# Kernel tuning notes

Measured on AMD Instinct MI355X. Metric: run time of the kernel, lower is better.

## Reference

```python
import jax, jax.numpy as jnp
import numpy as np

DIM = 1024
GROUP = 16
N_LIN = 18   # 6 blocks * 3 quantized linears
N_LN = 5
RANK = 32
BATCH = 32768


def _dequant(q, s):
    # q: [DIM, DIM] int values in [0,16); s: [DIM*DIM/GROUP] per-group scales
    w = (q.reshape(-1, GROUP).astype(jnp.float32) - 8.0) * s[:, None]
    return w.reshape(DIM, DIM)


def _qlora_linear(x, q, s, b, la, lb):
    # x: [N, DIM]; la: [RANK, DIM]; lb: [DIM, RANK]
    w = _dequant(q, s)
    base = x @ w.T + b
    lora = (x @ la.T) @ lb.T
    return base + lora


def _layernorm(x, g, b):
    m = jnp.mean(x, axis=-1, keepdims=True)
    v = jnp.var(x, axis=-1, keepdims=True)
    return (x - m) / jnp.sqrt(v + 1e-5) * g + b


def setup_inputs() -> dict:
    key = jax.random.key(0)
    ks = jax.random.split(key, 8)
    x = jax.random.normal(ks[0], (BATCH, DIM), dtype=jnp.float32)
    wq = jax.random.randint(ks[1], (N_LIN, DIM, DIM), 0, 16, dtype=jnp.int32)
    scales = jax.random.uniform(ks[2], (N_LIN, DIM * DIM // GROUP), dtype=jnp.float32) * 0.02 + 1e-3
    bias = jax.random.normal(ks[3], (N_LIN, DIM), dtype=jnp.float32) * 0.02
    lora_a = jax.random.normal(ks[4], (N_LIN, RANK, DIM), dtype=jnp.float32) * 0.05
    lora_b = jax.random.normal(ks[5], (N_LIN, DIM, RANK), dtype=jnp.float32) * 0.05
    gamma = jnp.ones((N_LN, DIM), dtype=jnp.float32)
    beta = jnp.zeros((N_LN, DIM), dtype=jnp.float32)
    return {"x": x, "wq": wq, "scales": scales, "bias": bias,
            "lora_a": lora_a, "lora_b": lora_b, "gamma": gamma, "beta": beta}


def reference(x, wq, scales, bias, lora_a, lora_b, gamma, beta):
    h = x.astype(jnp.float32)
    li = 0
    for blk in range(6):
        r = h
        for j in range(3):
            h = _qlora_linear(h, wq[li], scales[li], bias[li], lora_a[li], lora_b[li])
            li += 1
            if j < 2:
                h = jax.nn.relu(h)
        h = h + r
        if blk < 5:
            h = _layernorm(h, gamma[blk], beta[blk])
    return h
```

## Files before the change

### kernel.cpp

```cpp
#include <hip/hip_runtime.h>

typedef unsigned int u32;
typedef unsigned short u16;
typedef _Float16 f16;
typedef f16 f16x8 __attribute__((ext_vector_type(8)));
typedef float f32x4 __attribute__((ext_vector_type(4)));
typedef u16 u16x8 __attribute__((ext_vector_type(8)));

#define DIM 1024
#define BATCH 32768
#define RANK 32
#define NLIN 18

__device__ __forceinline__ u16 f2h(float f) {
    f16 h = (f16)f;
    return *(u16*)&h;
}
__device__ __forceinline__ float h2f(u16 u) {
    f16 h;
    *(u16*)&h = u;
    return (float)h;
}

__device__ __forceinline__ void gload16(const u16* g, u16* l) {
    __builtin_amdgcn_global_load_lds((__attribute__((address_space(1))) const void*)g,
                                     (__attribute__((address_space(3))) void*)l,
                                     16, 0, 0);
}

#define BAR()        __builtin_amdgcn_s_barrier()
#define SB0()        __builtin_amdgcn_sched_barrier(0)
#define ASM_VM0()    asm volatile("s_waitcnt vmcnt(0)" ::: "memory")
#define ASM_VM4()    asm volatile("s_waitcnt vmcnt(4)" ::: "memory")
#define ASM_VM8()    asm volatile("s_waitcnt vmcnt(8)" ::: "memory")
#define ASM_LG0()    asm volatile("s_waitcnt lgkmcnt(0)" ::: "memory")

__global__ __launch_bounds__(256) void build_weff(
    const int* __restrict__ wq, const float* __restrict__ scales,
    const float* __restrict__ la, const float* __restrict__ lb,
    u16* __restrict__ weff)
{
    const int rb = blockIdx.x;
    const int li = blockIdx.y;
    const int tid = threadIdx.x;
    const int row0 = rb * 16;
    const int* wqL = wq + (size_t)li * DIM * DIM;
    const float* sL = scales + (size_t)li * (DIM * DIM / 16);
    const float* laL = la + (size_t)li * RANK * DIM;
    const float* lbL = lb + (size_t)li * DIM * RANK;
    u16* wout = weff + (size_t)li * DIM * DIM;

    for (int kc = 0; kc < 4; ++kc) {
        const int k = kc * 256 + tid;
        float lar[RANK];
        #pragma unroll
        for (int r = 0; r < RANK; ++r) lar[r] = laL[r * DIM + k];
        const int ks = k >> 4;
        #pragma unroll
        for (int og = 0; og < 16; og += 4) {
            const int m0 = row0 + og;
            float a0 = ((float)wqL[(m0 + 0) * DIM + k] - 8.0f) * sL[((m0 + 0) << 6) + ks];
            float a1 = ((float)wqL[(m0 + 1) * DIM + k] - 8.0f) * sL[((m0 + 1) << 6) + ks];
            float a2 = ((float)wqL[(m0 + 2) * DIM + k] - 8.0f) * sL[((m0 + 2) << 6) + ks];
            float a3 = ((float)wqL[(m0 + 3) * DIM + k] - 8.0f) * sL[((m0 + 3) << 6) + ks];
            #pragma unroll
            for (int r = 0; r < RANK; ++r) {
                const float lv = lar[r];
                a0 += lbL[(m0 + 0) * RANK + r] * lv;
                a1 += lbL[(m0 + 1) * RANK + r] * lv;
                a2 += lbL[(m0 + 2) * RANK + r] * lv;
                a3 += lbL[(m0 + 3) * RANK + r] * lv;
            }
            wout[(m0 + 0) * DIM + k] = f2h(a0);
            wout[(m0 + 1) * DIM + k] = f2h(a1);
            wout[(m0 + 2) * DIM + k] = f2h(a2);
            wout[(m0 + 3) * DIM + k] = f2h(a3);
        }
    }
}

__global__ __launch_bounds__(256) void xcast(const float* __restrict__ x, u16* __restrict__ o) {
    size_t i = ((size_t)blockIdx.x * 256 + threadIdx.x) * 8;
    float4 a = *(const float4*)(x + i);
    float4 b = *(const float4*)(x + i + 4);
    u16x8 v;
    v[0] = f2h(a.x); v[1] = f2h(a.y); v[2] = f2h(a.z); v[3] = f2h(a.w);
    v[4] = f2h(b.x); v[5] = f2h(b.y); v[6] = f2h(b.z); v[7] = f2h(b.w);
    *(u16x8*)(o + i) = v;
}

template<int EPI>
__global__ __launch_bounds__(512, 2) void gemm256(
    const u16* __restrict__ X, const u16* __restrict__ W,
    const float* __restrict__ bias, const u16* __restrict__ res,
    void* __restrict__ outp)
{
    __shared__ __align__(16) u16 As3[3 * 16384];
    __shared__ __align__(16) u16 Bs[2 * 16384];
    const int tid = threadIdx.x;
    const int bid = blockIdx.x;
    const int wg = (bid & 7) * 64 + (bid >> 3);
    const int bm = wg >> 2;
    const int bn = wg & 3;
    const int wid = tid >> 6;
    const int lane = tid & 63;
    const int wm = wid >> 2;
    const int wn = wid & 3;

    const int c1 = tid, c2 = tid + 512;
    const int r1 = c1 >> 3, r2 = c2 >> 3;
    const int l1 = ((c1 & 7) ^ (r1 & 7)) * 8;
    const int l2 = ((c2 & 7) ^ (r2 & 7)) * 8;
    const u16* gA0a = X + (size_t)(bm * 256 +       r1) * DIM + l1;
    const u16* gA0b = X + (size_t)(bm * 256 +       r2) * DIM + l2;
    const u16* gA1a = X + (size_t)(bm * 256 + 128 + r1) * DIM + l1;
    const u16* gA1b = X + (size_t)(bm * 256 + 128 + r2) * DIM + l2;
    const u16* gB0a = W + (size_t)(bn * 256 +       r1) * DIM + l1;
    const u16* gB0b = W + (size_t)(bn * 256 +       r2) * DIM + l2;
    const u16* gB1a = W + (size_t)(bn * 256 + 128 + r1) * DIM + l1;
    const u16* gB1b = W + (size_t)(bn * 256 + 128 + r2) * DIM + l2;
    const int d1 = c1 * 8, d2 = c2 * 8;

    const int kg = lane >> 4;
    const int sw = lane & 7;
    const int ch0 = ((0 * 4 + kg) ^ sw) * 8;
    const int ch1 = ((1 * 4 + kg) ^ sw) * 8;
    const int aoff = (wm * 128 + (lane & 15)) * 64;
    const int boff = (wn * 64 + (lane & 15)) * 64;

    f32x4 acc[8][4];
    #pragma unroll
    for (int i = 0; i < 8; ++i)
        #pragma unroll
        for (int j = 0; j < 4; ++j)
            acc[i][j] = (f32x4){0.f, 0.f, 0.f, 0.f};
    f16x8 af[4][2];
    f16x8 bf[4][2];

    gload16(gA0a, &As3[d1]);        gload16(gA0b, &As3[d2]);
    gload16(gA1a, &As3[8192 + d1]); gload16(gA1b, &As3[8192 + d2]);
    gload16(gB0a, &Bs[d1]);         gload16(gB0b, &Bs[d2]);
    gload16(gB1a, &Bs[8192 + d1]);  gload16(gB1b, &Bs[8192 + d2]);
    gload16(gA0a + 64, &As3[16384 + d1]);        gload16(gA0b + 64, &As3[16384 + d2]);
    gload16(gA1a + 64, &As3[16384 + 8192 + d1]); gload16(gA1b + 64, &As3[16384 + 8192 + d2]);
    gload16(gB0a + 64, &Bs[16384 + d1]);         gload16(gB0b + 64, &Bs[16384 + d2]);
    gload16(gB1a + 64, &Bs[16384 + 8192 + d1]);  gload16(gB1b + 64, &Bs[16384 + 8192 + d2]);

    #define RD_A(MH, BUF) { \
        _Pragma("unroll") \
        for (int fm = 0; fm < 4; ++fm) { \
            af[fm][0] = *(const f16x8*)&(BUF)[aoff + ((MH)*64 + fm*16)*64 + ch0]; \
            af[fm][1] = *(const f16x8*)&(BUF)[aoff + ((MH)*64 + fm*16)*64 + ch1]; \
        } }
    #define RD_B(BUF) { \
        _Pragma("unroll") \
        for (int fn = 0; fn < 4; ++fn) { \
            bf[fn][0] = *(const f16x8*)&(BUF)[boff + (fn*16)*64 + ch0]; \
            bf[fn][1] = *(const f16x8*)&(BUF)[boff + (fn*16)*64 + ch1]; \
        } }
    #define QUAD(MH, NH) { \
        __builtin_amdgcn_s_setprio(1); \
        _Pragma("unroll") \
        for (int ks = 0; ks < 2; ++ks) \
            _Pragma("unroll") \
            for (int fm = 0; fm < 4; ++fm) \
                _Pragma("unroll") \
                for (int fn = 0; fn < 2; ++fn) \
                    acc[(MH)*4+fm][(NH)*2+fn] = __builtin_amdgcn_mfma_f32_16x16x32_f16( \
                        af[fm][ks], bf[(NH)*2+fn][ks], acc[(MH)*4+fm][(NH)*2+fn], 0, 0, 0); \
        __builtin_amdgcn_s_setprio(0); }

    ASM_VM8();
    BAR();
    RD_A(0, (&As3[0]));
    RD_B((&Bs[0]));

    int aCur = 0, aNext = 16384, aWr = 32768;
    int bCur = 0, bNext = 16384;
    #pragma unroll 1
    for (int t = 0; t < 16; ++t) {
        const int ko2 = (t + 2) * 64;
        if (t <= 13) {
            gload16(gA0a + ko2, &As3[aWr + d1]);        gload16(gA0b + ko2, &As3[aWr + d2]);
            gload16(gA1a + ko2, &As3[aWr + 8192 + d1]); gload16(gA1b + ko2, &As3[aWr + 8192 + d2]);
        }
        ASM_LG0(); SB0();
        QUAD(0, 0); QUAD(0, 1);
        RD_A(1, (&As3[aCur]));
        if (t <= 13) ASM_VM4(); else if (t == 14) ASM_VM0();
        BAR();
        if (t <= 13) {
            gload16(gB0a + ko2, &Bs[bCur + d1]);        gload16(gB0b + ko2, &Bs[bCur + d2]);
            gload16(gB1a + ko2, &Bs[bCur + 8192 + d1]); gload16(gB1b + ko2, &Bs[bCur + 8192 + d2]);
        }
        ASM_LG0(); SB0();
        QUAD(1, 0); QUAD(1, 1);
        if (t <= 14) {
            RD_A(0, (&As3[aNext]));
            RD_B((&Bs[bNext]));
        }
        BAR();
        int tmp = aCur; aCur = aNext; aNext = aWr; aWr = tmp;
        tmp = bCur; bCur = bNext; bNext = tmp;
    }

    float* blk = (float*)&As3[0] + wid * 1088;
    const int mrow = bm * 256 + wm * 128;
    const int ncol = bn * 256 + wn * 64 + (lane & 7) * 8;
    float4 bv0 = *(const float4*)&bias[ncol];
    float4 bv1 = *(const float4*)&bias[ncol + 4];
    #pragma unroll
    for (int fm = 0; fm < 8; ++fm) {
        __builtin_amdgcn_sched_barrier(0);
        #pragma unroll
        for (int fn = 0; fn < 4; ++fn)
            #pragma unroll
            for (int reg = 0; reg < 4; ++reg)
                blk[((lane >> 4) * 4 + reg) * 68 + (lane & 15) + fn * 16] = acc[fm][fn][reg];
        ASM_LG0();
        __builtin_amdgcn_sched_barrier(0);
        #pragma unroll
        for (int pass = 0; pass < 2; ++pass) {
            const float* rp = &blk[(pass * 8 + (lane >> 3)) * 68 + (lane & 7) * 8];
            float4 v0 = *(const float4*)rp;
            float4 v1 = *(const float4*)(rp + 4);
            v0.x += bv0.x; v0.y += bv0.y; v0.z += bv0.z; v0.w += bv0.w;
            v1.x += bv1.x; v1.y += bv1.y; v1.z += bv1.z; v1.w += bv1.w;
            const int m = mrow + fm * 16 + pass * 8 + (lane >> 3);
            const size_t gi = (size_t)m * DIM + ncol;
            if (EPI == 0) {
                u16x8 o;
                o[0] = f2h(fmaxf(v0.x, 0.f)); o[1] = f2h(fmaxf(v0.y, 0.f));
                o[2] = f2h(fmaxf(v0.z, 0.f)); o[3] = f2h(fmaxf(v0.w, 0.f));
                o[4] = f2h(fmaxf(v1.x, 0.f)); o[5] = f2h(fmaxf(v1.y, 0.f));
                o[6] = f2h(fmaxf(v1.z, 0.f)); o[7] = f2h(fmaxf(v1.w, 0.f));
                *(u16x8*)((u16*)outp + gi) = o;
            } else {
                u16x8 rv = *(const u16x8*)(res + gi);
                v0.x += h2f(rv[0]); v0.y += h2f(rv[1]); v0.z += h2f(rv[2]); v0.w += h2f(rv[3]);
                v1.x += h2f(rv[4]); v1.y += h2f(rv[5]); v1.z += h2f(rv[6]); v1.w += h2f(rv[7]);
                if (EPI == 1) {
                    u16x8 o;
                    o[0] = f2h(v0.x); o[1] = f2h(v0.y); o[2] = f2h(v0.z); o[3] = f2h(v0.w);
                    o[4] = f2h(v1.x); o[5] = f2h(v1.y); o[6] = f2h(v1.z); o[7] = f2h(v1.w);
                    *(u16x8*)((u16*)outp + gi) = o;
                } else {
                    *(float4*)((float*)outp + gi) = v0;
                    *(float4*)((float*)outp + gi + 4) = v1;
                }
            }
        }
        ASM_LG0();
    }
    #undef RD_A
    #undef RD_B
    #undef QUAD
}

__global__ __launch_bounds__(256) void ln_k(const u16* __restrict__ in,
    const float* __restrict__ g, const float* __restrict__ b, u16* __restrict__ out)
{
    int row = blockIdx.x * 4 + (threadIdx.x >> 6);
    int lane = threadIdx.x & 63;
    const u16* rp = in + (size_t)row * DIM;
    u16x8 v0 = *(const u16x8*)(rp + lane * 8);
    u16x8 v1 = *(const u16x8*)(rp + 512 + lane * 8);
    float f[16];
    #pragma unroll
    for (int j = 0; j < 8; ++j) { f[j] = h2f(v0[j]); f[8 + j] = h2f(v1[j]); }
    float s = 0.f, sq = 0.f;
    #pragma unroll
    for (int j = 0; j < 16; ++j) { s += f[j]; sq += f[j] * f[j]; }
    #pragma unroll
    for (int m = 1; m < 64; m <<= 1) { s += __shfl_xor(s, m); sq += __shfl_xor(sq, m); }
    float mean = s * (1.0f / 1024.0f);
    float var = sq * (1.0f / 1024.0f) - mean * mean;
    float rstd = 1.0f / sqrtf(var + 1e-5f);
    u16x8 o0, o1;
    #pragma unroll
    for (int j = 0; j < 8; ++j) {
        int c0 = lane * 8 + j, c1 = 512 + lane * 8 + j;
        o0[j] = f2h((f[j] - mean) * rstd * g[c0] + b[c0]);
        o1[j] = f2h((f[8 + j] - mean) * rstd * g[c1] + b[c1]);
    }
    u16* op = out + (size_t)row * DIM;
    *(u16x8*)(op + lane * 8) = o0;
    *(u16x8*)(op + 512 + lane * 8) = o1;
}

extern "C" void kernel_launch(void* const* d_in, const int* in_sizes, int n_in,
                              void* d_out, int out_size, void* d_ws, size_t ws_size,
                              hipStream_t stream) {
    const float* x      = (const float*)d_in[0];
    const int*   wq     = (const int*)d_in[1];
    const float* scales = (const float*)d_in[2];
    const float* bias   = (const float*)d_in[3];
    const float* la     = (const float*)d_in[4];
    const float* lb     = (const float*)d_in[5];
    const float* gamma  = (const float*)d_in[6];
    const float* beta   = (const float*)d_in[7];

    char* ws = (char*)d_ws;
    u16* Weff = (u16*)ws;
    u16* actA = (u16*)(ws + (size_t)NLIN * DIM * DIM * 2);
    u16* actB = actA + (size_t)BATCH * DIM;
    u16* dob  = (u16*)d_out;
    float* dof = (float*)d_out;

    build_weff<<<dim3(64, 18), 256, 0, stream>>>(wq, scales, la, lb, Weff);
    xcast<<<(BATCH * DIM) / 2048, 256, 0, stream>>>(x, actA);

    int li = 0;
    for (int blk = 0; blk < 6; ++blk) {
        const u16* w0 = Weff + (size_t)(li + 0) * DIM * DIM;
        const u16* w1 = Weff + (size_t)(li + 1) * DIM * DIM;
        const u16* w2 = Weff + (size_t)(li + 2) * DIM * DIM;
        const float* b0 = bias + (li + 0) * DIM;
        const float* b1 = bias + (li + 1) * DIM;
        const float* b2 = bias + (li + 2) * DIM;
        if (blk < 5) {
            gemm256<0><<<512, 512, 0, stream>>>(actA, w0, b0, nullptr, actB);
            gemm256<0><<<512, 512, 0, stream>>>(actB, w1, b1, nullptr, dob);
            gemm256<1><<<512, 512, 0, stream>>>(dob,  w2, b2, actA, actB);
            ln_k<<<BATCH / 4, 256, 0, stream>>>(actB, gamma + blk * DIM, beta + blk * DIM, actA);
        } else {
            gemm256<0><<<512, 512, 0, stream>>>(actA, w0, b0, nullptr, dob);
            gemm256<0><<<512, 512, 0, stream>>>(dob,  w1, b1, nullptr, actB);
            gemm256<2><<<512, 512, 0, stream>>>(actB, w2, b2, actA, (void*)dof);
        }
        li += 3;
    }
}
```

Baseline: 1.467 ms.

## Interleave global-to-LDS loads and split B-fragment reads across MFMA quadrants

Restructures the GEMM main loop so the global-to-LDS loads for the next tile are spread across the four MFMA quadrants in pairs, each separated by barriers, instead of issued in two bursts. The B fragment read is split into two halves, and the second half is issued at the start of each iteration so it overlaps with compute. Wait counts move to finer values (vmcnt 6, lgkmcnt 4) so compute can start before all LDS reads land. This is meant to smooth memory-issue pressure and hide latency, at the cost of many more workgroup barriers per iteration.

```diff
diff --git a/kernel.cpp b/kernel.cpp
--- a/kernel.cpp
+++ b/kernel.cpp
@@ -31,9 +31,10 @@
 #define BAR()        __builtin_amdgcn_s_barrier()
 #define SB0()        __builtin_amdgcn_sched_barrier(0)
 #define ASM_VM0()    asm volatile("s_waitcnt vmcnt(0)" ::: "memory")
-#define ASM_VM4()    asm volatile("s_waitcnt vmcnt(4)" ::: "memory")
+#define ASM_VM6()    asm volatile("s_waitcnt vmcnt(6)" ::: "memory")
 #define ASM_VM8()    asm volatile("s_waitcnt vmcnt(8)" ::: "memory")
 #define ASM_LG0()    asm volatile("s_waitcnt lgkmcnt(0)" ::: "memory")
+#define ASM_LG4()    asm volatile("s_waitcnt lgkmcnt(4)" ::: "memory")
 
 __global__ __launch_bounds__(256) void build_weff(
     const int* __restrict__ wq, const float* __restrict__ scales,
@@ -137,24 +138,21 @@
     f16x8 af[4][2];
     f16x8 bf[4][2];
 
-    gload16(gA0a, &As3[d1]);        gload16(gA0b, &As3[d2]);
-    gload16(gA1a, &As3[8192 + d1]); gload16(gA1b, &As3[8192 + d2]);
-    gload16(gB0a, &Bs[d1]);         gload16(gB0b, &Bs[d2]);
-    gload16(gB1a, &Bs[8192 + d1]);  gload16(gB1b, &Bs[8192 + d2]);
-    gload16(gA0a + 64, &As3[16384 + d1]);        gload16(gA0b + 64, &As3[16384 + d2]);
-    gload16(gA1a + 64, &As3[16384 + 8192 + d1]); gload16(gA1b + 64, &As3[16384 + 8192 + d2]);
-    gload16(gB0a + 64, &Bs[16384 + d1]);         gload16(gB0b + 64, &Bs[16384 + d2]);
-    gload16(gB1a + 64, &Bs[16384 + 8192 + d1]);  gload16(gB1b + 64, &Bs[16384 + 8192 + d2]);
-
     #define RD_A(MH, BUF) { \
         _Pragma("unroll") \
         for (int fm = 0; fm < 4; ++fm) { \
             af[fm][0] = *(const f16x8*)&(BUF)[aoff + ((MH)*64 + fm*16)*64 + ch0]; \
             af[fm][1] = *(const f16x8*)&(BUF)[aoff + ((MH)*64 + fm*16)*64 + ch1]; \
         } }
-    #define RD_B(BUF) { \
+    #define RD_B01(BUF) { \
         _Pragma("unroll") \
-        for (int fn = 0; fn < 4; ++fn) { \
+        for (int fn = 0; fn < 2; ++fn) { \
+            bf[fn][0] = *(const f16x8*)&(BUF)[boff + (fn*16)*64 + ch0]; \
+            bf[fn][1] = *(const f16x8*)&(BUF)[boff + (fn*16)*64 + ch1]; \
+        } }
+    #define RD_B23(BUF) { \
+        _Pragma("unroll") \
+        for (int fn = 2; fn < 4; ++fn) { \
             bf[fn][0] = *(const f16x8*)&(BUF)[boff + (fn*16)*64 + ch0]; \
             bf[fn][1] = *(const f16x8*)&(BUF)[boff + (fn*16)*64 + ch1]; \
         } }
@@ -170,40 +168,66 @@
                         af[fm][ks], bf[(NH)*2+fn][ks], acc[(MH)*4+fm][(NH)*2+fn], 0, 0, 0); \
         __builtin_amdgcn_s_setprio(0); }
 
+    gload16(gA0a, &As3[d1]);        gload16(gA0b, &As3[d2]);
+    gload16(gA1a, &As3[8192 + d1]); gload16(gA1b, &As3[8192 + d2]);
+    gload16(gB0a, &Bs[d1]);         gload16(gB0b, &Bs[d2]);
+    gload16(gB1a, &Bs[8192 + d1]);  gload16(gB1b, &Bs[8192 + d2]);
+    gload16(gA0a + 64, &As3[16384 + d1]);        gload16(gA0b + 64, &As3[16384 + d2]);
+    gload16(gA1a + 64, &As3[16384 + 8192 + d1]); gload16(gA1b + 64, &As3[16384 + 8192 + d2]);
+    gload16(gB0a + 64, &Bs[16384 + d1]);         gload16(gB0b + 64, &Bs[16384 + d2]);
+    gload16(gB1a + 64, &Bs[16384 + 8192 + d1]);  gload16(gB1b + 64, &Bs[16384 + 8192 + d2]);
+
     ASM_VM8();
     BAR();
     RD_A(0, (&As3[0]));
-    RD_B((&Bs[0]));
+    RD_B01((&Bs[0]));
+    SB0();
 
     int aCur = 0, aNext = 16384, aWr = 32768;
     int bCur = 0, bNext = 16384;
     #pragma unroll 1
     for (int t = 0; t < 16; ++t) {
         const int ko2 = (t + 2) * 64;
-        if (t <= 13) {
-            gload16(gA0a + ko2, &As3[aWr + d1]);        gload16(gA0b + ko2, &As3[aWr + d2]);
-            gload16(gA1a + ko2, &As3[aWr + 8192 + d1]); gload16(gA1b + ko2, &As3[aWr + 8192 + d2]);
-        }
-        ASM_LG0(); SB0();
-        QUAD(0, 0); QUAD(0, 1);
+        const bool st = (t <= 13);
+        RD_B23((&Bs[bCur]));
+        if (st) { gload16(gA0a + ko2, &As3[aWr + d1]); gload16(gA0b + ko2, &As3[aWr + d2]); }
+        SB0();
+        BAR();
+        ASM_LG4();
+        QUAD(0, 0);
+        SB0();
+        BAR();
+        if (st) { gload16(gA1a + ko2, &As3[aWr + 8192 + d1]); gload16(gA1b + ko2, &As3[aWr + 8192 + d2]); }
+        SB0();
+        BAR();
+        ASM_LG0();
+        QUAD(0, 1);
         RD_A(1, (&As3[aCur]));
-        if (t <= 13) ASM_VM4(); else if (t == 14) ASM_VM0();
-        BAR();
-        if (t <= 13) {
-            gload16(gB0a + ko2, &Bs[bCur + d1]);        gload16(gB0b + ko2, &Bs[bCur + d2]);
-            gload16(gB1a + ko2, &Bs[bCur + 8192 + d1]); gload16(gB1b + ko2, &Bs[bCur + 8192 + d2]);
-        }
-        ASM_LG0(); SB0();
-        QUAD(1, 0); QUAD(1, 1);
+        SB0();
+        BAR();
+        if (st) { gload16(gB0a + ko2, &Bs[bCur + d1]); gload16(gB0b + ko2, &Bs[bCur + d2]); }
+        if (st) ASM_VM6(); else if (t == 14) ASM_VM0();
+        SB0();
+        BAR();
+        ASM_LG0();
+        QUAD(1, 0);
+        SB0();
+        BAR();
+        if (st) { gload16(gB1a + ko2, &Bs[bCur + 8192 + d1]); gload16(gB1b + ko2, &Bs[bCur + 8192 + d2]); }
+        SB0();
+        BAR();
+        QUAD(1, 1);
         if (t <= 14) {
             RD_A(0, (&As3[aNext]));
-            RD_B((&Bs[bNext]));
+            RD_B01((&Bs[bNext]));
         }
+        SB0();
         BAR();
         int tmp = aCur; aCur = aNext; aNext = aWr; aWr = tmp;
         tmp = bCur; bCur = bNext; bNext = tmp;
     }
 
+    ASM_LG0();
     float* blk = (float*)&As3[0] + wid * 1088;
     const int mrow = bm * 256 + wm * 128;
     const int ncol = bn * 256 + wn * 64 + (lane & 7) * 8;
@@ -253,7 +277,8 @@
         ASM_LG0();
     }
     #undef RD_A
-    #undef RD_B
+    #undef RD_B01
+    #undef RD_B23
     #undef QUAD
 }
 
```

New measurement: 1.574 ms. +7.3%, slower.
